# Kernel tuning notes

Measured on AMD Instinct MI355X. Metric: run time of the kernel, lower is better.

## Reference

```python
import jax, jax.numpy as jnp
import numpy as np

NUM_HEADS = 8

def setup_inputs() -> dict:
    key = jax.random.key(0)
    ks = jax.random.split(key, 12)
    B, C, H, W = 4, 256, 64, 64
    QK = 256
    NSP = 256
    x = jax.random.normal(ks[0], (B, C, H, W), dtype=jnp.float32)
    affinity_matrix = jax.random.uniform(ks[1], (B, NSP, H * W), dtype=jnp.float32)
    norm_w = 1.0 + 0.02 * jax.random.normal(ks[2], (C,), dtype=jnp.float32)
    norm_b = 0.02 * jax.random.normal(ks[3], (C,), dtype=jnp.float32)
    Wq = 0.02 * jax.random.normal(ks[4], (QK, C), dtype=jnp.float32)
    Wk = 0.02 * jax.random.normal(ks[5], (QK, C), dtype=jnp.float32)
    Wv = 0.02 * jax.random.normal(ks[6], (C, C), dtype=jnp.float32)
    Wsp = 0.02 * jax.random.normal(ks[7], (QK, C), dtype=jnp.float32)
    lepe_w = 0.02 * jax.random.normal(ks[8], (C, 1, 3, 3), dtype=jnp.float32)  # depthwise OIHW
    lepe_b = 0.02 * jax.random.normal(ks[9], (C,), dtype=jnp.float32)
    return {"x": x, "affinity_matrix": affinity_matrix, "norm_w": norm_w,
            "norm_b": norm_b, "Wq": Wq, "Wk": Wk, "Wv": Wv, "Wsp": Wsp,
            "lepe_w": lepe_w, "lepe_b": lepe_b, "num_spixels": NSP}


def _layernorm2d(x, w, b, eps=1e-6):
    # LayerNorm over channel dim of NCHW input
    xp = x.transpose(0, 2, 3, 1)  # B,H,W,C
    mu = xp.mean(-1, keepdims=True)
    var = ((xp - mu) ** 2).mean(-1, keepdims=True)
    xn = (xp - mu) * jax.lax.rsqrt(var + eps) * w + b
    return xn.transpose(0, 3, 1, 2)


def _sgca(x, affinity_matrix, norm_w, norm_b, Wq, Wk, Wv, Wsp, lepe_w, lepe_b, num_spixels):
    B, C, H, W = x.shape
    HW = H * W
    h = NUM_HEADS
    qk_dim = Wq.shape[0]
    dqk = qk_dim // h
    dv = C // h
    scale = (C // h) ** -0.5

    xn = _layernorm2d(x, norm_w, norm_b)

    # superpixel aggregation: b (hw) c
    x_flat = xn.reshape(B, C, HW).transpose(0, 2, 1)  # B,HW,C
    stoken = jnp.einsum('bmn,bnc->bmc', affinity_matrix, x_flat)
    stoken = stoken / (affinity_matrix.sum(-1, keepdims=True) + 1e-16)  # B,nsp,C

    # sp projection -> B,h,dqk,nsp
    st = jnp.einsum('bmc,qc->bmq', stoken, Wsp).transpose(0, 2, 1)
    st = st.reshape(B, h, dqk, num_spixels)

    # 1x1 conv projections
    q = jnp.einsum('oc,bchw->bohw', Wq, xn).reshape(B, h, dqk, HW)
    k = jnp.einsum('oc,bchw->bohw', Wk, xn).reshape(B, h, dqk, HW)
    vx = jnp.einsum('oc,bchw->bohw', Wv, xn)  # B,C,H,W
    v = vx.reshape(B, h, dv, HW)

    # LePE: depthwise 3x3 conv on v(x)
    lepe = jax.lax.conv_general_dilated(
        vx, lepe_w, window_strides=(1, 1), padding=((1, 1), (1, 1)),
        feature_group_count=C, dimension_numbers=('NCHW', 'OIHW', 'NCHW'))
    lepe = lepe + lepe_b[None, :, None, None]
    # faithful to original: [B,C,HW] -> permute -> [B,HW,C] -> reshape B,C,H,W
    lepe = lepe.reshape(B, C, HW).transpose(0, 2, 1).reshape(B, C, H, W)

    # stage 1: k^T @ stoken, softmax over HW axis
    s_attn = jnp.einsum('bhdn,bhdm->bhnm', k, st) * scale  # B,h,HW,nsp
    s_attn = jax.nn.softmax(s_attn, axis=-2)
    s_out = jnp.einsum('bhdn,bhnm->bhdm', v, s_attn)  # B,h,dv,nsp

    # stage 2: stoken^T @ q, softmax over nsp axis
    x_attn = jnp.einsum('bhdm,bhdn->bhmn', st, q) * scale  # B,h,nsp,HW
    x_attn = jax.nn.softmax(x_attn, axis=-2)
    x_out = jnp.einsum('bhdm,bhmn->bhdn', s_out, x_attn).reshape(B, C, H, W)

    return x_out + lepe


def reference(x, affinity_matrix, norm_w, norm_b, Wq, Wk, Wv, Wsp, lepe_w, lepe_b, num_spixels):
    return _sgca(x, affinity_matrix, norm_w, norm_b, Wq, Wk, Wv, Wsp, lepe_w, lepe_b, num_spixels)
```

## Files before the change

### kernel.cpp

```cpp
#include <hip/hip_runtime.h>
#include <hip/hip_bf16.h>

#define BATCH 4
#define CCH   256
#define HWHW  4096
#define NSP   256
#define NHEAD 8
#define SCALE 0.17677669529663689f
#define PLANE 1048576L

typedef short bf16x8 __attribute__((ext_vector_type(8)));
typedef short bf16x4 __attribute__((ext_vector_type(4)));
typedef float f32x4  __attribute__((ext_vector_type(4)));

__device__ __forceinline__ short f2bs(float f) {
    __hip_bfloat16 h = __float2bfloat16(f);
    return *(short*)&h;
}
__device__ __forceinline__ bf16x8 cvt8(float4 a, float4 b) {
    bf16x8 p;
    p[0] = f2bs(a.x); p[1] = f2bs(a.y); p[2] = f2bs(a.z); p[3] = f2bs(a.w);
    p[4] = f2bs(b.x); p[5] = f2bs(b.y); p[6] = f2bs(b.z); p[7] = f2bs(b.w);
    return p;
}
__device__ __forceinline__ void gll16(const __hip_bfloat16* g, __hip_bfloat16* l) {
    __builtin_amdgcn_global_load_lds(
        (const __attribute__((address_space(1))) unsigned int*)(const void*)g,
        (__attribute__((address_space(3))) unsigned int*)(void*)l,
        16, 0, 0);
}

__global__ __launch_bounds__(512)
void ln_fused_kernel(const float* __restrict__ x, const float* __restrict__ w,
                     const float* __restrict__ bb,
                     const float* __restrict__ Wq, const float* __restrict__ Wk,
                     const float* __restrict__ Wv, const float* __restrict__ Wsp,
                     __hip_bfloat16* __restrict__ xn_cn,
                     __hip_bfloat16* __restrict__ xn_nc,
                     __hip_bfloat16* __restrict__ wbf)
{
    __shared__ float ps[32][64], pss[32][64];
    __shared__ float mus[64], rstds[64];
    __shared__ float wls[256], bls[256];
    int blk = blockIdx.x;
    int t = threadIdx.x;
    if (blk >= 256) {
        int sel = blk - 256;
        const float* src = (sel == 0) ? Wq : (sel == 1) ? Wk : (sel == 2) ? Wv : Wsp;
        __hip_bfloat16* dst = wbf + sel * 65536;
        for (int i = t * 4; i < 65536; i += 2048) {
            float4 f = *(const float4*)(src + i);
            __hip_bfloat16 p[4];
            p[0] = __float2bfloat16(f.x); p[1] = __float2bfloat16(f.y);
            p[2] = __float2bfloat16(f.z); p[3] = __float2bfloat16(f.w);
            *(int2*)(dst + i) = *(int2*)p;
        }
        return;
    }
    int b = blk >> 6;
    int n0 = (blk & 63) * 64;
    int pg = t & 15;
    int cq = t >> 4;
    if (t < 256) { wls[t] = w[t]; bls[t] = bb[t]; }

    const float* xp = x + ((long)(b * CCH + cq * 8)) * HWHW + n0 + pg * 4;
    float4 v[8];
#pragma unroll
    for (int i = 0; i < 8; ++i) v[i] = *(const float4*)(xp + (long)i * HWHW);
    float4 s = {0.f,0.f,0.f,0.f}, ss = {0.f,0.f,0.f,0.f};
#pragma unroll
    for (int i = 0; i < 8; ++i) {
        s.x += v[i].x; s.y += v[i].y; s.z += v[i].z; s.w += v[i].w;
        ss.x += v[i].x * v[i].x; ss.y += v[i].y * v[i].y;
        ss.z += v[i].z * v[i].z; ss.w += v[i].w * v[i].w;
    }
    *(float4*)&ps[cq][pg * 4]  = s;
    *(float4*)&pss[cq][pg * 4] = ss;
    __syncthreads();
    if (t < 64) {
        float S = 0.f, SS = 0.f;
#pragma unroll
        for (int q = 0; q < 32; ++q) { S += ps[q][t]; SS += pss[q][t]; }
        float mu = S * (1.f / 256.f);
        float var = SS * (1.f / 256.f) - mu * mu;
        mus[t] = mu; rstds[t] = rsqrtf(var + 1e-6f);
    }
    __syncthreads();
    float4 mu4 = *(float4*)&mus[pg * 4];
    float4 rs4 = *(float4*)&rstds[pg * 4];

    bf16x8 pk[4];
#pragma unroll
    for (int i = 0; i < 8; ++i) {
        int c = cq * 8 + i;
        float wc = wls[c], bc = bls[c];
        short h0 = f2bs((v[i].x - mu4.x) * rs4.x * wc + bc);
        short h1 = f2bs((v[i].y - mu4.y) * rs4.y * wc + bc);
        short h2 = f2bs((v[i].z - mu4.z) * rs4.z * wc + bc);
        short h3 = f2bs((v[i].w - mu4.w) * rs4.w * wc + bc);
        pk[0][i] = h0; pk[1][i] = h1; pk[2][i] = h2; pk[3][i] = h3;
        bf16x4 q; q[0] = h0; q[1] = h1; q[2] = h2; q[3] = h3;
        *(bf16x4*)(xn_cn + ((long)(b * CCH + c)) * HWHW + n0 + pg * 4) = q;
    }
#pragma unroll
    for (int j = 0; j < 4; ++j)
        *(bf16x8*)(xn_nc + ((long)b * HWHW + n0 + pg * 4 + j) * CCH + cq * 8) = pk[j];
}

__device__ __forceinline__ void gemm_k256_128(
    const __hip_bfloat16* __restrict__ A, const __hip_bfloat16* __restrict__ B,
    __hip_bfloat16* __restrict__ C, int bx, int by, int bz,
    int N, long aStrideZ, long bStrideZ, long cStrideZ,
    __hip_bfloat16* __restrict__ Asm)
{
    const int K = 256;
    const int t = threadIdx.x, lane = t & 63, w = t >> 6;
    const int l15 = lane & 15, quad = lane >> 4;
    const int Mt = by * 128, Nt = bx * 128;
    {
        const __hip_bfloat16* aBase = A + (long)bz * aStrideZ
            + (long)(Mt + l15) * K + quad * 8;
#pragma unroll
        for (int p = 0; p < 16; ++p) {
            const int rt = w * 2 + (p >> 3), s = p & 7;
            gll16(aBase + (long)(rt * 16) * K + s * 32, Asm + (rt * 8 + s) * 512);
        }
    }
    const int wm2 = w & 1, wn2 = w >> 1;
    const __hip_bfloat16* bBase = B + (long)bz * bStrideZ
        + (long)(Nt + wn2 * 64 + l15) * K + quad * 8;

    f32x4 acc[4][4];
#pragma unroll
    for (int mi = 0; mi < 4; ++mi)
#pragma unroll
        for (int nj = 0; nj < 4; ++nj) acc[mi][nj] = f32x4{0.f,0.f,0.f,0.f};

    bf16x8 bEv[4], bOd[4];
#pragma unroll
    for (int nj = 0; nj < 4; ++nj)
        bEv[nj] = *(const bf16x8*)(bBase + (long)(nj * 16) * K);
    __syncthreads();
#pragma unroll
    for (int sp = 0; sp < 4; ++sp) {
        const int s0 = 2 * sp, s1 = 2 * sp + 1;
#pragma unroll
        for (int nj = 0; nj < 4; ++nj)
            bOd[nj] = *(const bf16x8*)(bBase + (long)(nj * 16) * K + s1 * 32);
#pragma unroll
        for (int mi = 0; mi < 4; ++mi) {
            bf16x8 a = *(const bf16x8*)&Asm[((wm2 * 4 + mi) * 8 + s0) * 512 + lane * 8];
            acc[mi][0] = __builtin_amdgcn_mfma_f32_16x16x32_bf16(a, bEv[0], acc[mi][0], 0, 0, 0);
            acc[mi][1] = __builtin_amdgcn_mfma_f32_16x16x32_bf16(a, bEv[1], acc[mi][1], 0, 0, 0);
            acc[mi][2] = __builtin_amdgcn_mfma_f32_16x16x32_bf16(a, bEv[2], acc[mi][2], 0, 0, 0);
            acc[mi][3] = __builtin_amdgcn_mfma_f32_16x16x32_bf16(a, bEv[3], acc[mi][3], 0, 0, 0);
        }
        if (sp < 3) {
#pragma unroll
            for (int nj = 0; nj < 4; ++nj)
                bEv[nj] = *(const bf16x8*)(bBase + (long)(nj * 16) * K + (s0 + 2) * 32);
        }
#pragma unroll
        for (int mi = 0; mi < 4; ++mi) {
            bf16x8 a = *(const bf16x8*)&Asm[((wm2 * 4 + mi) * 8 + s1) * 512 + lane * 8];
            acc[mi][0] = __builtin_amdgcn_mfma_f32_16x16x32_bf16(a, bOd[0], acc[mi][0], 0, 0, 0);
            acc[mi][1] = __builtin_amdgcn_mfma_f32_16x16x32_bf16(a, bOd[1], acc[mi][1], 0, 0, 0);
            acc[mi][2] = __builtin_amdgcn_mfma_f32_16x16x32_bf16(a, bOd[2], acc[mi][2], 0, 0, 0);
            acc[mi][3] = __builtin_amdgcn_mfma_f32_16x16x32_bf16(a, bOd[3], acc[mi][3], 0, 0, 0);
        }
    }
#pragma unroll
    for (int mi = 0; mi < 4; ++mi)
#pragma unroll
        for (int nj = 0; nj < 4; ++nj)
#pragma unroll
            for (int r = 0; r < 4; ++r) {
                int m = Mt + wm2 * 64 + mi * 16 + quad * 4 + r;
                int n = Nt + wn2 * 64 + nj * 16 + l15;
                C[(long)bz * cStrideZ + (long)m * N + n] =
                    __float2bfloat16(acc[mi][nj][r]);
            }
}

template <int OUTK, int ASTAGE, bool ROWSUM, int NTL>
__device__ __forceinline__ void gemm_body(
    const void* __restrict__ Av, const __hip_bfloat16* __restrict__ B,
    void* __restrict__ Cptr, int bx, int by, int bz,
    int N, int K, int kChunk, int kShift,
    long aStrideZ, long bStrideZ, long cStrideZ,
    float* __restrict__ rsPart,
    __hip_bfloat16* __restrict__ Asm, __hip_bfloat16* __restrict__ Bsm,
    float* __restrict__ rsl)
{
    int z = bz;
    int b = z >> kShift;
    int ch = z & ((1 << kShift) - 1);
    int t = threadIdx.x;
    int lane = t & 63, w = t >> 6;
    int l15 = lane & 15, quad = lane >> 4;
    int Mt = by * 64, Nt = bx * 64 * NTL;

    if (ASTAGE == 2 && t < 64) {
        float s = 0.f;
#pragma unroll
        for (int pl = 0; pl < 8; ++pl) s += rsPart[((b * 8 + pl) << 8) + Mt + t];
        rsl[t] = s;
    }

    long aOff = (long)b * aStrideZ + (long)ch * kChunk
        + (long)(Mt + w * 16 + l15) * K + quad * 8;
    const float* aSrcF = (const float*)Av + aOff;
    const __hip_bfloat16* bSrc = B + (long)b * bStrideZ + (long)ch * kChunk
        + (long)(Nt + w * 16 + l15) * K + quad * 8;

    f32x4 acc[NTL][2][2];
#pragma unroll
    for (int nt = 0; nt < NTL; ++nt)
#pragma unroll
        for (int i = 0; i < 2; ++i)
#pragma unroll
            for (int j = 0; j < 2; ++j) acc[nt][i][j] = f32x4{0.f,0.f,0.f,0.f};
    f32x4 rs0 = {0.f,0.f,0.f,0.f}, rs1 = rs0;
    bf16x8 onesf;
    { short o = (l15 == 0) ? (short)0x3F80 : (short)0;
      onesf = bf16x8{o, o, o, o, o, o, o, o}; }
    int wm = (w & 1) * 2, wn = (w >> 1) * 2;

    float4 pf0, pf1, pf2, pf3;
    if (ASTAGE == 1) {
        pf0 = *(const float4*)(aSrcF);      pf1 = *(const float4*)(aSrcF + 4);
        pf2 = *(const float4*)(aSrcF + 32); pf3 = *(const float4*)(aSrcF + 36);
    }

    const bf16x8* AsmU = (const bf16x8*)Asm;
    const bf16x8* BsmU = (const bf16x8*)Bsm;

    for (int k0 = 0; k0 < kChunk; k0 += 64) {
        if (ASTAGE == 1) {
            *(bf16x8*)&Asm[t * 8]        = cvt8(pf0, pf1);
            *(bf16x8*)&Asm[2048 + t * 8] = cvt8(pf2, pf3);
        } else {
#pragma unroll
            for (int kh = 0; kh < 2; ++kh) {
                float4 s0 = {0.f,0.f,0.f,0.f}, s1 = {0.f,0.f,0.f,0.f};
#pragma unroll
                for (int pl = 0; pl < 8; ++pl) {
                    const float* p = aSrcF + (long)pl * 65536 + k0 + kh * 32;
                    float4 u0 = *(const float4*)p, u1 = *(const float4*)(p + 4);
                    s0.x += u0.x; s0.y += u0.y; s0.z += u0.z; s0.w += u0.w;
                    s1.x += u1.x; s1.y += u1.y; s1.z += u1.z; s1.w += u1.w;
                }
                *(bf16x8*)&Asm[kh * 2048 + t * 8] = cvt8(s0, s1);
            }
        }
#pragma unroll
        for (int nt = 0; nt < NTL; ++nt) {
            gll16(bSrc + (long)nt * 64 * K + k0,      Bsm + nt * 4096 + w * 512);
            gll16(bSrc + (long)nt * 64 * K + k0 + 32, Bsm + nt * 4096 + 2048 + w * 512);
        }
        __syncthreads();
        if (ASTAGE == 1 && k0 + 64 < kChunk) {
            const float* nx = aSrcF + k0 + 64;
            pf0 = *(const float4*)nx;        pf1 = *(const float4*)(nx + 4);
            pf2 = *(const float4*)(nx + 32); pf3 = *(const float4*)(nx + 36);
        }
#pragma unroll
        for (int kh = 0; kh < 2; ++kh) {
            bf16x8 a0 = AsmU[kh * 256 + wm * 64 + lane];
            bf16x8 a1 = AsmU[kh * 256 + (wm + 1) * 64 + lane];
            if (ROWSUM) {
                rs0 = __builtin_amdgcn_mfma_f32_16x16x32_bf16(a0, onesf, rs0, 0, 0, 0);
                rs1 = __builtin_amdgcn_mfma_f32_16x16x32_bf16(a1, onesf, rs1, 0, 0, 0);
            }
#pragma unroll
            for (int nt = 0; nt < NTL; ++nt) {
                bf16x8 b0 = BsmU[nt * 512 + kh * 256 + wn * 64 + lane];
                bf16x8 b1 = BsmU[nt * 512 + kh * 256 + (wn + 1) * 64 + lane];
                acc[nt][0][0] = __builtin_amdgcn_mfma_f32_16x16x32_bf16(a0, b0, acc[nt][0][0], 0, 0, 0);
                acc[nt][0][1] = __builtin_amdgcn_mfma_f32_16x16x32_bf16(a0, b1, acc[nt][0][1], 0, 0, 0);
                acc[nt][1][0] = __builtin_amdgcn_mfma_f32_16x16x32_bf16(a1, b0, acc[nt][1][0], 0, 0, 0);
                acc[nt][1][1] = __builtin_amdgcn_mfma_f32_16x16x32_bf16(a1, b1, acc[nt][1][1], 0, 0, 0);
            }
        }
        __syncthreads();
    }
    if (ROWSUM && bx == 0 && (w >> 1) == 0 && l15 == 0) {
#pragma unroll
        for (int r = 0; r < 4; ++r) {
            rsPart[(long)z * 256 + Mt + wm * 16 + quad * 4 + r]       = rs0[r];
            rsPart[(long)z * 256 + Mt + (wm + 1) * 16 + quad * 4 + r] = rs1[r];
        }
    }
#pragma unroll
    for (int nt = 0; nt < NTL; ++nt)
#pragma unroll
        for (int i = 0; i < 2; ++i)
#pragma unroll
            for (int j = 0; j < 2; ++j)
#pragma unroll
                for (int r = 0; r < 4; ++r) {
                    int m = Mt + (wm + i) * 16 + quad * 4 + r;
                    int n = Nt + nt * 64 + (wn + j) * 16 + l15;
                    float val = acc[nt][i][j][r];
                    if (ASTAGE == 2) val /= (rsl[m - Mt] + 1e-16f);
                    long off = (long)z * cStrideZ + (long)m * N + n;
                    if (OUTK == 0) ((float*)Cptr)[off] = val;
                    else ((__hip_bfloat16*)Cptr)[off] = __float2bfloat16(val);
                }
}

__global__ __launch_bounds__(256, 2)
void mega1_kernel(const float* __restrict__ aff,
                  const __hip_bfloat16* __restrict__ xn_cn,
                  const __hip_bfloat16* __restrict__ xn_nc,
                  const __hip_bfloat16* __restrict__ wbf,
                  __hip_bfloat16* __restrict__ qk_nc,
                  __hip_bfloat16* __restrict__ v_cn,
                  float* __restrict__ stoken_part,
                  float* __restrict__ rs_part)
{
    __shared__ __align__(16) char smem[65536];
    __hip_bfloat16* Asm = (__hip_bfloat16*)smem;
    __hip_bfloat16* Bsm = (__hip_bfloat16*)(smem + 8192);
    __hip_bfloat16* A128 = (__hip_bfloat16*)smem;
    int blk = blockIdx.x;
    if (blk < 128) {
        int i = blk;
        gemm_body<0, 1, true, 4>(aff, xn_cn, stoken_part,
            0, i >> 5, i & 31, 256, 4096, 512, 3,
            PLANE, PLANE, 65536L, rs_part, Asm, Bsm, nullptr);
    } else if (blk < 640) {
        int i = blk - 128;
        int bx = i >> 7, rem = i & 127;
        gemm_k256_128(xn_nc, wbf, qk_nc,
            bx, rem >> 2, rem & 3, 512, PLANE, 0L, 2 * PLANE, A128);
    } else {
        int i = blk - 640;
        int by = i >> 7, rem = i & 127;
        gemm_k256_128(wbf + 2 * 65536, xn_nc, v_cn,
            rem >> 2, by, rem & 3, 4096, 0L, PLANE, PLANE, A128);
    }
}

__device__ __forceinline__
void lepe_dev(char* smem, int bx, int cy, int b,
              const __hip_bfloat16* __restrict__ v_cn,
              const float* __restrict__ lw, const float* __restrict__ lb,
              __hip_bfloat16* __restrict__ lepe_cn)
{
    __hip_bfloat16* in_t    = (__hip_bfloat16*)smem;
    __hip_bfloat16* tile_bf = (__hip_bfloat16*)(smem + 24576);
    float* wls = (float*)(smem + 41472);
    float* bls = (float*)(smem + 42624);
    const int c0 = cy * 32;
    const int t = threadIdx.x;
    const int n0 = bx * 256, r0 = bx * 4;

    for (int i = t; i < 288; i += 256) wls[i] = lw[c0 * 9 + i];
    if (t < 32)  bls[t] = lb[c0 + t];
#pragma unroll
    for (int i = 0; i < 6; ++i) {
        int vi = t + i * 256;
        int ch = vi / 48;
        int off = (vi % 48) * 8;
        int g = (r0 - 1) * 64 + off;
        int4 val = {0, 0, 0, 0};
        if ((unsigned)g < 4096u)
            val = *(const int4*)(v_cn + (((long)(b * CCH + c0 + ch)) << 12) + g);
        *(int4*)&in_t[ch * 384 + off] = val;
    }
    __syncthreads();

    const int lane = t & 63, w = t >> 6;
#pragma unroll
    for (int i = 0; i < 8; ++i) {
        int ch = w * 8 + i;
        float cr[6], lf[6], rf[6];
#pragma unroll
        for (int rr = 0; rr < 6; ++rr) {
            cr[rr] = (float)in_t[ch * 384 + rr * 64 + lane];
            float lv = __shfl_up(cr[rr], 1);
            float rv = __shfl_down(cr[rr], 1);
            lf[rr] = (lane == 0) ? 0.f : lv;
            rf[rr] = (lane == 63) ? 0.f : rv;
        }
        float w0 = wls[ch*9+0], w1 = wls[ch*9+1], w2 = wls[ch*9+2];
        float w3 = wls[ch*9+3], w4 = wls[ch*9+4], w5 = wls[ch*9+5];
        float w6 = wls[ch*9+6], w7 = wls[ch*9+7], w8 = wls[ch*9+8];
        float bias = bls[ch];
#pragma unroll
        for (int r = 0; r < 4; ++r) {
            float acc = bias
                + lf[r]   * w0 + cr[r]   * w1 + rf[r]   * w2
                + lf[r+1] * w3 + cr[r+1] * w4 + rf[r+1] * w5
                + lf[r+2] * w6 + cr[r+2] * w7 + rf[r+2] * w8;
            tile_bf[(r * 64 + lane) * 33 + ch] = __float2bfloat16(acc);
        }
    }
    __syncthreads();
#pragma unroll
    for (int i = 0; i < 32; ++i) {
        int idx = t + i * 256;
        int nl = idx >> 5, cj = idx & 31;
        int sp = n0 + nl;
        lepe_cn[((long)(b * CCH + (sp >> 4)) << 12) + (nl & 15) * 256 + c0 + cj] =
            tile_bf[nl * 33 + cj];
    }
}

__global__ __launch_bounds__(256)
void stmd_lepe_kernel(const float* __restrict__ part,
                      const __hip_bfloat16* __restrict__ wsp,
                      __hip_bfloat16* __restrict__ st_md,
                      float* __restrict__ rs_part,
                      const __hip_bfloat16* __restrict__ v_cn,
                      const float* __restrict__ lw, const float* __restrict__ lb,
                      __hip_bfloat16* __restrict__ lepe_cn)
{
    __shared__ __align__(16) char smem[43008];
    int blk = blockIdx.x;
    if (blk < 64) {
        __hip_bfloat16* Asm = (__hip_bfloat16*)smem;
        __hip_bfloat16* Bsm = (__hip_bfloat16*)(smem + 8192);
        float* rsl = (float*)(smem + 16384);
        int i = blk;
        gemm_body<1, 2, false, 1>(part, wsp, st_md,
            i & 3, (i >> 2) & 3, i >> 4, 256, 256, 256, 0,
            524288L, 0L, 65536L, rs_part, Asm, Bsm, rsl);
    } else {
        int j = blk - 64;
        lepe_dev(smem, j & 15, (j >> 4) & 7, j >> 7, v_cn, lw, lb, lepe_cn);
    }
}

__global__ __launch_bounds__(256)
void mega2_kernel(const __hip_bfloat16* __restrict__ qk_nc,
                  const __hip_bfloat16* __restrict__ v_cn,
                  const __hip_bfloat16* __restrict__ st_md,
                  __hip_bfloat16* __restrict__ opart)
{
    __shared__ __align__(16) char smem[18432];
    __hip_bfloat16* Es  = (__hip_bfloat16*)smem;
    __hip_bfloat16* sts = (__hip_bfloat16*)smem;
    const int blk = blockIdx.x;
    const int mh = blk & 1;
    const int chunk = (blk >> 1) & 15;
    const int bh = blk >> 5;
    const int b = bh >> 3, h = bh & 7;
    const int t = threadIdx.x, lane = t & 63, w = t >> 6;
    const int l15 = lane & 15, quad = lane >> 4;
    const int n0 = chunk * 256;

    {
        int row = t >> 1, half = t & 1;
        const int4* src = (const int4*)(st_md
            + ((long)(b * 256 + mh * 128 + row)) * 256 + h * 32 + half * 16);
        int4* dst = (int4*)&sts[row * 40 + half * 16];
        dst[0] = src[0]; dst[1] = src[1];
    }
    const __hip_bfloat16* kfp = qk_nc + ((long)b * 4096 + n0 + 16 * w + l15) * 512 + 256 + h * 32 + quad * 8;
    const __hip_bfloat16* vp0 = v_cn + ((long)(b * 256 + h * 32 + l15)) * 4096 + n0 + quad * 8;
    const __hip_bfloat16* vp1 = vp0 + 16 * 4096;
    bf16x8 kfc = *(const bf16x8*)(kfp);
    __syncthreads();
    bf16x8 afrag[8];
#pragma unroll
    for (int mt = 0; mt < 8; ++mt)
        afrag[mt] = *(const bf16x8*)&sts[(mt * 16 + l15) * 40 + quad * 8];
    __syncthreads();
    bf16x8 onesf;
    { short o = (l15 == 0) ? (short)0x3F80 : (short)0;
      onesf = bf16x8{o, o, o, o, o, o, o, o}; }

    f32x4 occ[2][3];
#pragma unroll
    for (int i = 0; i < 2; ++i)
#pragma unroll
        for (int j = 0; j < 3; ++j) occ[i][j] = f32x4{0.f,0.f,0.f,0.f};

#pragma unroll
    for (int sub = 0; sub < 4; ++sub) {
        bf16x8 vv0 = *(const bf16x8*)(vp0 + sub * 64);
        bf16x8 vv1 = *(const bf16x8*)(vp1 + sub * 64);
        bf16x8 vv2 = *(const bf16x8*)(vp0 + sub * 64 + 32);
        bf16x8 vv3 = *(const bf16x8*)(vp1 + sub * 64 + 32);
#pragma unroll
        for (int mt = 0; mt < 8; ++mt) {
            f32x4 s = __builtin_amdgcn_mfma_f32_16x16x32_bf16(afrag[mt], kfc, f32x4{0.f,0.f,0.f,0.f}, 0, 0, 0);
#pragma unroll
            for (int r = 0; r < 4; ++r)
                Es[(mt * 16 + quad * 4 + r) * 72 + 16 * w + l15] =
                    __float2bfloat16(__expf(s[r] * SCALE));
        }
        if (sub < 3)
            kfc = *(const bf16x8*)(kfp + (long)(sub + 1) * 64 * 512);
        __syncthreads();
#pragma unroll
        for (int ks = 0; ks < 2; ++ks) {
            bf16x8 bf0 = (ks == 0) ? vv0 : vv2;
            bf16x8 bf1 = (ks == 0) ? vv1 : vv3;
#pragma unroll
            for (int mi = 0; mi < 2; ++mi) {
                bf16x8 af = *(const bf16x8*)&Es[(32 * w + mi * 16 + l15) * 72 + ks * 32 + quad * 8];
                occ[mi][0] = __builtin_amdgcn_mfma_f32_16x16x32_bf16(af, bf0, occ[mi][0], 0, 0, 0);
                occ[mi][1] = __builtin_amdgcn_mfma_f32_16x16x32_bf16(af, bf1, occ[mi][1], 0, 0, 0);
                occ[mi][2] = __builtin_amdgcn_mfma_f32_16x16x32_bf16(af, onesf, occ[mi][2], 0, 0, 0);
            }
        }
        __syncthreads();
    }
    __hip_bfloat16* tb = Es;
#pragma unroll
    for (int mi = 0; mi < 2; ++mi)
#pragma unroll
        for (int jt = 0; jt < 3; ++jt) {
            if (jt == 2 && l15 != 0) continue;
            int col = jt * 16 + l15;
#pragma unroll
            for (int r = 0; r < 4; ++r) {
                int m = 32 * w + mi * 16 + quad * 4 + r;
                tb[col * 136 + m] = __float2bfloat16(occ[mi][jt][r]);
            }
        }
    __syncthreads();
    int* og = (int*)(opart) + (long)(chunk * 32 + bh) * 4224;
    const int* tbi = (const int*)tb;
#pragma unroll
    for (int i = 0; i < 9; ++i) {
        int idx = t + i * 256;
        if (idx < 2112) {
            int row = idx >> 6, off = idx & 63;
            og[row * 128 + mh * 64 + off] = tbi[row * 68 + off];
        }
    }
}

__global__ __launch_bounds__(256)
void merge1_kernel(const __hip_bfloat16* __restrict__ opart, __hip_bfloat16* __restrict__ sout)
{
    int t = blockIdx.x * 256 + threadIdx.x;
    int m = t & 255;
    int d = (t >> 8) & 31;
    int bh = t >> 13;
    float num = 0.f, den = 0.f;
    for (int ch = 0; ch < 16; ++ch) {
        long base = (long)((ch * 32 + bh) * 33) * 256 + m;
        num += (float)opart[base + (long)d * 256];
        den += (float)opart[base + 32 * 256];
    }
    sout[(long)bh * 8192 + d * 256 + m] = __float2bfloat16(num / den);
}

__global__ __launch_bounds__(256)
void stage2_mfma(const __hip_bfloat16* __restrict__ qk_nc,
                 const __hip_bfloat16* __restrict__ st_md,
                 const __hip_bfloat16* __restrict__ sout_bf,
                 const __hip_bfloat16* __restrict__ lepe_cn,
                 float* __restrict__ out)
{
    __shared__ __align__(16) char smem[50688];
    __hip_bfloat16* Es2 = (__hip_bfloat16*)smem;
    __hip_bfloat16* sos = (__hip_bfloat16*)(smem + 33792);
    float* o_t = (float*)smem;
    const int chunk = blockIdx.x, bh = blockIdx.y;
    const int b = bh >> 3, h = bh & 7;
    const int t = threadIdx.x, lane = t & 63, w = t >> 6;
    const int l15 = lane & 15, quad = lane >> 4;
    const int n0 = chunk * 128;

    {
        int row = t >> 3, seg = t & 7;
        const int4* src = (const int4*)(sout_bf + (long)bh * 8192 + row * 256 + seg * 32);
        int4* dst = (int4*)&sos[row * 264 + seg * 32];
        dst[0] = src[0]; dst[1] = src[1]; dst[2] = src[2]; dst[3] = src[3];
    }
    bf16x8 stfrag[4];
#pragma unroll
    for (int mt = 0; mt < 4; ++mt)
        stfrag[mt] = *(const bf16x8*)(st_md
            + ((long)(b * 256 + 64 * w + mt * 16 + l15)) * 256 + h * 32 + quad * 8);
    const __hip_bfloat16* qfp = qk_nc + ((long)b * 4096 + n0 + l15) * 512 + h * 32 + quad * 8;
    bf16x8 qq[2][4];
#pragma unroll
    for (int nt = 0; nt < 4; ++nt)
        qq[0][nt] = *(const bf16x8*)(qfp + (long)(nt * 16) * 512);
    bf16x8 onesf;
    { short o = (l15 == 0) ? (short)0x3F80 : (short)0;
      onesf = bf16x8{o, o, o, o, o, o, o, o}; }
    __syncthreads();

#pragma unroll
    for (int sub = 0; sub < 2; ++sub) {
        const int nbase = n0 + sub * 64;
#pragma unroll
        for (int nt = 0; nt < 4; ++nt) {
            bf16x8 qf = qq[sub][nt];
#pragma unroll
            for (int mt = 0; mt < 4; ++mt) {
                f32x4 s = __builtin_amdgcn_mfma_f32_16x16x32_bf16(qf, stfrag[mt], f32x4{0.f,0.f,0.f,0.f}, 0, 0, 0);
#pragma unroll
                for (int r = 0; r < 4; ++r)
                    Es2[(nt * 16 + quad * 4 + r) * 264 + 64 * w + mt * 16 + l15] =
                        __float2bfloat16(__expf(s[r] * SCALE));
            }
        }
        if (sub < 1) {
#pragma unroll
            for (int nt = 0; nt < 4; ++nt)
                qq[1][nt] = *(const bf16x8*)(qfp + (long)(64 + nt * 16) * 512);
        }
        __syncthreads();
        f32x4 o0 = {0.f,0.f,0.f,0.f}, o1 = o0, o2 = o0;
#pragma unroll
        for (int ks = 0; ks < 8; ++ks) {
            bf16x8 af = *(const bf16x8*)&Es2[(16 * w + l15) * 264 + ks * 32 + quad * 8];
            bf16x8 b0 = *(const bf16x8*)&sos[(l15) * 264 + ks * 32 + quad * 8];
            bf16x8 b1 = *(const bf16x8*)&sos[(16 + l15) * 264 + ks * 32 + quad * 8];
            o0 = __builtin_amdgcn_mfma_f32_16x16x32_bf16(af, b0, o0, 0, 0, 0);
            o1 = __builtin_amdgcn_mfma_f32_16x16x32_bf16(af, b1, o1, 0, 0, 0);
            o2 = __builtin_amdgcn_mfma_f32_16x16x32_bf16(af, onesf, o2, 0, 0, 0);
        }
        __syncthreads();
#pragma unroll
        for (int r = 0; r < 4; ++r) {
            float den = __shfl(o2[r], lane & 48);
            float inv = 1.f / den;
            o_t[(l15) * 68 + 16 * w + quad * 4 + r]      = o0[r] * inv;
            o_t[(16 + l15) * 68 + 16 * w + quad * 4 + r] = o1[r] * inv;
        }
        __syncthreads();
        {
            int row = t >> 3, coff = (t & 7) * 8;
            long gb = ((long)(b * 256 + h * 32 + row)) * 4096 + nbase + coff;
            int4 lp4 = *(const int4*)(lepe_cn + gb);
            const __hip_bfloat16* lp = (const __hip_bfloat16*)&lp4;
            const float* sp = &o_t[row * 68 + coff];
            float4 r0, r1;
            r0.x = sp[0] + (float)lp[0]; r0.y = sp[1] + (float)lp[1];
            r0.z = sp[2] + (float)lp[2]; r0.w = sp[3] + (float)lp[3];
            r1.x = sp[4] + (float)lp[4]; r1.y = sp[5] + (float)lp[5];
            r1.z = sp[6] + (float)lp[6]; r1.w = sp[7] + (float)lp[7];
            *(float4*)(out + gb)     = r0;
            *(float4*)(out + gb + 4) = r1;
        }
        __syncthreads();
    }
}

extern "C" void kernel_launch(void* const* d_in, const int* in_sizes, int n_in,
                              void* d_out, int out_size, void* d_ws, size_t ws_size,
                              hipStream_t stream)
{
    const float* x    = (const float*)d_in[0];
    const float* aff  = (const float*)d_in[1];
    const float* nw   = (const float*)d_in[2];
    const float* nb   = (const float*)d_in[3];
    const float* Wq   = (const float*)d_in[4];
    const float* Wk   = (const float*)d_in[5];
    const float* Wv   = (const float*)d_in[6];
    const float* Wsp  = (const float*)d_in[7];
    const float* lw   = (const float*)d_in[8];
    const float* lb   = (const float*)d_in[9];
    float* out = (float*)d_out;

    float* ws = (float*)d_ws;
    const long P = PLANE;
    __hip_bfloat16* qk_nc  = (__hip_bfloat16*)(ws);
    __hip_bfloat16* v_cn   = (__hip_bfloat16*)(ws + 4 * P);
    __hip_bfloat16* xn_cn  = (__hip_bfloat16*)(ws + 6 * P);
    __hip_bfloat16* xn_nc  = (__hip_bfloat16*)(ws + 8 * P);
    __hip_bfloat16* lepe_cn= (__hip_bfloat16*)(ws + 10 * P);
    float* stoken_part = ws + 14 * P;
    __hip_bfloat16* opart = (__hip_bfloat16*)(ws + 16 * P);
    float* tail        = ws + 16 * P + 2162688;
    __hip_bfloat16* wbf       = (__hip_bfloat16*)tail;
    __hip_bfloat16* st_md     = (__hip_bfloat16*)(tail + 262144);
    __hip_bfloat16* sout_bf   = (__hip_bfloat16*)(tail + 393216);
    float* rs_part = tail + 525312;

    ln_fused_kernel<<<260, 512, 0, stream>>>(x, nw, nb, Wq, Wk, Wv, Wsp,
                                             xn_cn, xn_nc, wbf);
    mega1_kernel<<<896, 256, 0, stream>>>(aff, xn_cn, xn_nc, wbf,
                                          qk_nc, v_cn, stoken_part, rs_part);
    stmd_lepe_kernel<<<576, 256, 0, stream>>>(stoken_part, wbf + 3 * 65536,
                                              st_md, rs_part,
                                              v_cn, lw, lb, lepe_cn);
    mega2_kernel<<<1024, 256, 0, stream>>>(qk_nc, v_cn, st_md, opart);
    merge1_kernel<<<1024, 256, 0, stream>>>(opart, sout_bf);
    stage2_mfma<<<dim3(32, 32), 256, 0, stream>>>(qk_nc, st_md, sout_bf, lepe_cn, out);
}
```

Measured before the change: 187.6 us.

## Fold sp-projection into mega1 via atomic counter; merge merge1 with LePE

The stoken superpixel projection GEMM now runs as 64 extra blocks inside mega1. These blocks spin on a device-scope atomic counter until all 128 stoken-partial blocks have signalled completion. The counter is reset in the LayerNorm kernel. The separate merge1 kernel is merged with the LePE depthwise conv into a single launch, and the merge is vectorised to 4 bf16 per thread. Together this removes one kernel launch and overlaps the projection with the q/k/v GEMMs. The cost is a spin-wait that assumes the producer blocks get scheduled first, with a bounded guard against deadlock, and LePE now runs after mega2 instead of before it.

```diff
diff --git a/kernel.cpp b/kernel.cpp
--- a/kernel.cpp
+++ b/kernel.cpp
@@ -17,6 +17,9 @@
     __hip_bfloat16 h = __float2bfloat16(f);
     return *(short*)&h;
 }
+__device__ __forceinline__ float bs2f(short s) {
+    __hip_bfloat16 h; *(short*)&h = s; return (float)h;
+}
 __device__ __forceinline__ bf16x8 cvt8(float4 a, float4 b) {
     bf16x8 p;
     p[0] = f2bs(a.x); p[1] = f2bs(a.y); p[2] = f2bs(a.z); p[3] = f2bs(a.w);
@@ -37,7 +40,8 @@
                      const float* __restrict__ Wv, const float* __restrict__ Wsp,
                      __hip_bfloat16* __restrict__ xn_cn,
                      __hip_bfloat16* __restrict__ xn_nc,
-                     __hip_bfloat16* __restrict__ wbf)
+                     __hip_bfloat16* __restrict__ wbf,
+                     unsigned* __restrict__ cnt)
 {
     __shared__ float ps[32][64], pss[32][64];
     __shared__ float mus[64], rstds[64];
@@ -46,6 +50,8 @@
     int t = threadIdx.x;
     if (blk >= 256) {
         int sel = blk - 256;
+        if (sel == 0 && t == 0)
+            __hip_atomic_store(cnt, 0u, __ATOMIC_RELAXED, __HIP_MEMORY_SCOPE_AGENT);
         const float* src = (sel == 0) ? Wq : (sel == 1) ? Wk : (sel == 2) ? Wv : Wsp;
         __hip_bfloat16* dst = wbf + sel * 65536;
         for (int i = t * 4; i < 65536; i += 2048) {
@@ -317,11 +323,14 @@
                   __hip_bfloat16* __restrict__ qk_nc,
                   __hip_bfloat16* __restrict__ v_cn,
                   float* __restrict__ stoken_part,
-                  float* __restrict__ rs_part)
+                  float* __restrict__ rs_part,
+                  __hip_bfloat16* __restrict__ st_md,
+                  unsigned* __restrict__ cnt)
 {
     __shared__ __align__(16) char smem[65536];
     __hip_bfloat16* Asm = (__hip_bfloat16*)smem;
     __hip_bfloat16* Bsm = (__hip_bfloat16*)(smem + 8192);
+    float* rslS = (float*)(smem + 16384);
     __hip_bfloat16* A128 = (__hip_bfloat16*)smem;
     int blk = blockIdx.x;
     if (blk < 128) {
@@ -329,16 +338,33 @@
         gemm_body<0, 1, true, 4>(aff, xn_cn, stoken_part,
             0, i >> 5, i & 31, 256, 4096, 512, 3,
             PLANE, PLANE, 65536L, rs_part, Asm, Bsm, nullptr);
+        __syncthreads();
+        if (threadIdx.x == 0) {
+            __threadfence();
+            __hip_atomic_fetch_add(cnt, 1u, __ATOMIC_RELEASE, __HIP_MEMORY_SCOPE_AGENT);
+        }
     } else if (blk < 640) {
         int i = blk - 128;
         int bx = i >> 7, rem = i & 127;
         gemm_k256_128(xn_nc, wbf, qk_nc,
             bx, rem >> 2, rem & 3, 512, PLANE, 0L, 2 * PLANE, A128);
-    } else {
+    } else if (blk < 896) {
         int i = blk - 640;
         int by = i >> 7, rem = i & 127;
         gemm_k256_128(wbf + 2 * 65536, xn_nc, v_cn,
             rem >> 2, by, rem & 3, 4096, 0L, PLANE, PLANE, A128);
+    } else {
+        if (threadIdx.x == 0) {
+            long guard = 0;
+            while (__hip_atomic_load(cnt, __ATOMIC_ACQUIRE, __HIP_MEMORY_SCOPE_AGENT) < 128u
+                   && ++guard < (1L << 22))
+                __builtin_amdgcn_s_sleep(8);
+        }
+        __syncthreads();
+        int i = blk - 896;
+        gemm_body<1, 2, false, 1>(stoken_part, wbf + 3 * 65536, st_md,
+            i & 3, (i >> 2) & 3, i >> 4, 256, 256, 256, 0,
+            524288L, 0L, 65536L, rs_part, Asm, Bsm, rslS);
     }
 }
 
@@ -409,26 +435,37 @@
 }
 
 __global__ __launch_bounds__(256)
-void stmd_lepe_kernel(const float* __restrict__ part,
-                      const __hip_bfloat16* __restrict__ wsp,
-                      __hip_bfloat16* __restrict__ st_md,
-                      float* __restrict__ rs_part,
-                      const __hip_bfloat16* __restrict__ v_cn,
-                      const float* __restrict__ lw, const float* __restrict__ lb,
-                      __hip_bfloat16* __restrict__ lepe_cn)
+void merge_lepe_kernel(const __hip_bfloat16* __restrict__ opart,
+                       __hip_bfloat16* __restrict__ sout,
+                       const __hip_bfloat16* __restrict__ v_cn,
+                       const float* __restrict__ lw, const float* __restrict__ lb,
+                       __hip_bfloat16* __restrict__ lepe_cn)
 {
     __shared__ __align__(16) char smem[43008];
     int blk = blockIdx.x;
-    if (blk < 64) {
-        __hip_bfloat16* Asm = (__hip_bfloat16*)smem;
-        __hip_bfloat16* Bsm = (__hip_bfloat16*)(smem + 8192);
-        float* rsl = (float*)(smem + 16384);
-        int i = blk;
-        gemm_body<1, 2, false, 1>(part, wsp, st_md,
-            i & 3, (i >> 2) & 3, i >> 4, 256, 256, 256, 0,
-            524288L, 0L, 65536L, rs_part, Asm, Bsm, rsl);
+    if (blk < 256) {
+        int t = blk * 256 + threadIdx.x;
+        int mq = (t & 63) * 4;
+        int d  = (t >> 6) & 31;
+        int bh = t >> 11;
+        float num[4] = {0.f,0.f,0.f,0.f}, den[4] = {0.f,0.f,0.f,0.f};
+#pragma unroll
+        for (int ch = 0; ch < 16; ++ch) {
+            long base = (long)((ch * 32 + bh) * 33) * 256 + mq;
+            bf16x4 nv = *(const bf16x4*)(opart + base + (long)d * 256);
+            bf16x4 dv = *(const bf16x4*)(opart + base + 8192);
+#pragma unroll
+            for (int j = 0; j < 4; ++j) {
+                num[j] += bs2f(nv[j]);
+                den[j] += bs2f(dv[j]);
+            }
+        }
+        bf16x4 o;
+#pragma unroll
+        for (int j = 0; j < 4; ++j) o[j] = f2bs(num[j] / den[j]);
+        *(bf16x4*)(sout + (long)bh * 8192 + d * 256 + mq) = o;
     } else {
-        int j = blk - 64;
+        int j = blk - 256;
         lepe_dev(smem, j & 15, (j >> 4) & 7, j >> 7, v_cn, lw, lb, lepe_cn);
     }
 }
@@ -533,22 +570,6 @@
             og[row * 128 + mh * 64 + off] = tbi[row * 68 + off];
         }
     }
-}
-
-__global__ __launch_bounds__(256)
-void merge1_kernel(const __hip_bfloat16* __restrict__ opart, __hip_bfloat16* __restrict__ sout)
-{
-    int t = blockIdx.x * 256 + threadIdx.x;
-    int m = t & 255;
-    int d = (t >> 8) & 31;
-    int bh = t >> 13;
-    float num = 0.f, den = 0.f;
-    for (int ch = 0; ch < 16; ++ch) {
-        long base = (long)((ch * 32 + bh) * 33) * 256 + m;
-        num += (float)opart[base + (long)d * 256];
-        den += (float)opart[base + 32 * 256];
-    }
-    sout[(long)bh * 8192 + d * 256 + m] = __float2bfloat16(num / den);
 }
 
 __global__ __launch_bounds__(256)
@@ -676,16 +697,16 @@
     __hip_bfloat16* wbf       = (__hip_bfloat16*)tail;
     __hip_bfloat16* st_md     = (__hip_bfloat16*)(tail + 262144);
     __hip_bfloat16* sout_bf   = (__hip_bfloat16*)(tail + 393216);
+    unsigned* cnt = (unsigned*)(tail + 524288);
     float* rs_part = tail + 525312;
 
     ln_fused_kernel<<<260, 512, 0, stream>>>(x, nw, nb, Wq, Wk, Wv, Wsp,
-                                             xn_cn, xn_nc, wbf);
-    mega1_kernel<<<896, 256, 0, stream>>>(aff, xn_cn, xn_nc, wbf,
-                                          qk_nc, v_cn, stoken_part, rs_part);
-    stmd_lepe_kernel<<<576, 256, 0, stream>>>(stoken_part, wbf + 3 * 65536,
-                                              st_md, rs_part,
-                                              v_cn, lw, lb, lepe_cn);
+                                             xn_cn, xn_nc, wbf, cnt);
+    mega1_kernel<<<960, 256, 0, stream>>>(aff, xn_cn, xn_nc, wbf,
+                                          qk_nc, v_cn, stoken_part, rs_part,
+                                          st_md, cnt);
     mega2_kernel<<<1024, 256, 0, stream>>>(qk_nc, v_cn, st_md, opart);
-    merge1_kernel<<<1024, 256, 0, stream>>>(opart, sout_bf);
+    merge_lepe_kernel<<<768, 256, 0, stream>>>(opart, sout_bf,
+                                               v_cn, lw, lb, lepe_cn);
     stage2_mfma<<<dim3(32, 32), 256, 0, stream>>>(qk_nc, st_md, sout_bf, lepe_cn, out);
 }
```

Result: slower. 205.3 us (+9.5%).
